# Kernel optimization log

Measured on AMD Instinct MI355X. Metric: run time of the kernel, lower is better.

Reference implementation:

```python
import jax, jax.numpy as jnp
import numpy as np

D_IN = 1024
D_OUT = 1024
NUM_HEADS = 16
HEAD_DIM = D_OUT // NUM_HEADS


def setup_inputs() -> dict:
    key = jax.random.key(0)
    ks = jax.random.split(key, 6)
    s = 1.0 / np.sqrt(D_IN)
    x = jax.random.normal(ks[0], (2, 2048, D_IN), dtype=jnp.float32)
    Wq = jax.random.uniform(ks[1], (D_IN, D_OUT), jnp.float32, -s, s)
    Wk = jax.random.uniform(ks[2], (D_IN, D_OUT), jnp.float32, -s, s)
    Wv = jax.random.uniform(ks[3], (D_IN, D_OUT), jnp.float32, -s, s)
    Wo = jax.random.uniform(ks[4], (D_OUT, D_OUT), jnp.float32, -s, s)
    bo = jax.random.uniform(ks[5], (D_OUT,), jnp.float32, -s, s)
    return {"x": x, "Wq": Wq, "Wk": Wk, "Wv": Wv, "Wo": Wo, "bo": bo}


def reference(x, Wq, Wk, Wv, Wo, bo):
    b, T, _ = x.shape
    # projections -> [b, heads, T, head_dim]
    def split_heads(y):
        return y.reshape(b, T, NUM_HEADS, HEAD_DIM).transpose(0, 2, 1, 3)
    q = split_heads(x @ Wq)
    k = split_heads(x @ Wk)
    v = split_heads(x @ Wv)
    scores = jnp.einsum("bhqd,bhkd->bhqk", q, k)  # [b,h,T,T]
    causal = jnp.triu(jnp.ones((T, T), dtype=bool), k=1)
    scores = jnp.where(causal, -jnp.inf, scores)
    weights = jax.nn.softmax(scores / np.sqrt(HEAD_DIM), axis=-1)
    # dropout p=0.0 (eval) -> identity
    ctx = jnp.einsum("bhqk,bhkd->bhqd", weights, v)
    ctx = ctx.transpose(0, 2, 1, 3).reshape(b, T, D_OUT)
    return ctx @ Wo + bo
```

## Files before the change

### kernel.cpp

```cpp
#include <hip/hip_runtime.h>
#include <hip/hip_bf16.h>
#include <math.h>

using f32x4  = __attribute__((ext_vector_type(4)))  float;
using f32x16 = __attribute__((ext_vector_type(16))) float;
using s16x8  = __attribute__((ext_vector_type(8)))  short;
using s16x4  = __attribute__((ext_vector_type(4)))  short;

#define HD 64
#define NH 16
#define TT 2048
#define DIN 1024
#define NB 2
#define M_TOK (NB*TT)
#define PADK 40
#define PSTR 36

__device__ __forceinline__ ushort f2b(float f) {
  union { float f; unsigned u; } v; v.f = f;
  unsigned u = v.u;
  return (ushort)((u + 0x7FFFu + ((u >> 16) & 1u)) >> 16);
}

__device__ __forceinline__ unsigned cvt_pk_bf16(float lo, float hi) {
  unsigned r;
  asm("v_cvt_pk_bf16_f32 %0, %1, %2" : "=v"(r) : "v"(lo), "v"(hi));
  return r;
}

__global__ __launch_bounds__(256) void cvt_f32_bf16(const float* __restrict__ in,
                                                    ushort* __restrict__ out, int n8) {
  int i = blockIdx.x * 256 + threadIdx.x;
  if (i >= n8) return;
  const f32x4* p = (const f32x4*)(in + (size_t)i * 8);
  f32x4 a = p[0], b = p[1];
  s16x8 o;
  o[0]=(short)f2b(a[0]); o[1]=(short)f2b(a[1]); o[2]=(short)f2b(a[2]); o[3]=(short)f2b(a[3]);
  o[4]=(short)f2b(b[0]); o[5]=(short)f2b(b[1]); o[6]=(short)f2b(b[2]); o[7]=(short)f2b(b[3]);
  *(s16x8*)(out + (size_t)i * 8) = o;
}

__global__ __launch_bounds__(256) void transpose_cvt(const float* __restrict__ W,
                                                     ushort* __restrict__ Wt, int K, int N) {
  __shared__ float tile[32][33];
  int nb = blockIdx.x * 32, kb = blockIdx.y * 32;
  int tx = threadIdx.x & 31, ty = threadIdx.x >> 5;
  #pragma unroll
  for (int j = ty; j < 32; j += 8) tile[j][tx] = W[(size_t)(kb + j) * N + nb + tx];
  __syncthreads();
  #pragma unroll
  for (int j = ty; j < 32; j += 8) Wt[(size_t)(nb + j) * K + kb + tx] = f2b(tile[tx][j]);
}

__global__ __launch_bounds__(256) void gemm_qkv(const ushort* __restrict__ Xb,
                                                const ushort* __restrict__ Wt,
                                                ushort* __restrict__ Qb,
                                                ushort* __restrict__ Kb,
                                                ushort* __restrict__ Vt) {
  __shared__ ushort Al[128 * PADK];
  __shared__ ushort Bl[128 * PADK];
  int tid = threadIdx.x, lane = tid & 63, wid = tid >> 6;
  int wr = wid >> 1, wc = wid & 1, g = lane >> 4, c = lane & 15;
  int m0 = blockIdx.y * 128, n0 = blockIdx.x * 128;
  f32x4 acc[4][4] = {};
  for (int k0 = 0; k0 < DIN; k0 += 32) {
    __syncthreads();
    #pragma unroll
    for (int j = 0; j < 2; ++j) {
      int ci = tid + j * 256;
      int row = ci >> 2, part = ci & 3;
      *(s16x8*)&Al[row * PADK + part * 8] =
          *(const s16x8*)&Xb[(size_t)(m0 + row) * DIN + k0 + part * 8];
      *(s16x8*)&Bl[row * PADK + part * 8] =
          *(const s16x8*)&Wt[(size_t)(n0 + row) * DIN + k0 + part * 8];
    }
    __syncthreads();
    s16x8 af[4], bfr[4];
    #pragma unroll
    for (int i = 0; i < 4; ++i) {
      af[i]  = *(const s16x8*)&Al[(wr * 64 + i * 16 + c) * PADK + g * 8];
      bfr[i] = *(const s16x8*)&Bl[(wc * 64 + i * 16 + c) * PADK + g * 8];
    }
    #pragma unroll
    for (int i = 0; i < 4; ++i)
      #pragma unroll
      for (int jn = 0; jn < 4; ++jn)
        acc[i][jn] = __builtin_amdgcn_mfma_f32_16x16x32_bf16(af[i], bfr[jn], acc[i][jn], 0, 0, 0);
  }
  #pragma unroll
  for (int i = 0; i < 4; ++i)
    #pragma unroll
    for (int jn = 0; jn < 4; ++jn) {
      int mrow = m0 + wr * 64 + i * 16 + g * 4;
      int n = n0 + wc * 64 + jn * 16 + c;
      int b = mrow >> 11, t = mrow & (TT - 1);
      int which = n >> 10, nn = n & 1023, h = nn >> 6, d = nn & 63;
      size_t bh = (size_t)(b * NH + h);
      if (which == 2) {
        s16x4 pk;
        pk[0]=(short)f2b(acc[i][jn][0]); pk[1]=(short)f2b(acc[i][jn][1]);
        pk[2]=(short)f2b(acc[i][jn][2]); pk[3]=(short)f2b(acc[i][jn][3]);
        *(s16x4*)&Vt[(bh * HD + d) * TT + t] = pk;
      } else {
        float sc = (which == 0) ? 0.125f * 1.44269504f : 1.0f;
        ushort* dst = (which == 0) ? &Qb[(bh * TT + t) * HD + d]
                                   : &Kb[(bh * TT + t) * HD + d];
        #pragma unroll
        for (int r = 0; r < 4; ++r) dst[(size_t)r * HD] = f2b(acc[i][jn][r] * sc);
      }
    }
}

__global__ __launch_bounds__(256, 4) void attn_fwd(const ushort* __restrict__ Qb,
                                                   const ushort* __restrict__ Kb,
                                                   const ushort* __restrict__ Vt,
                                                   ushort* __restrict__ Ctx) {
  __shared__ __align__(16) char smem[11264];
  int bh = blockIdx.y;
  int qc = (gridDim.x - 1) - blockIdx.x;
  int q0 = qc * 32;
  const ushort* Qh = Qb + (size_t)bh * TT * HD;
  const ushort* Kh = Kb + (size_t)bh * TT * HD;
  const ushort* Vh = Vt + (size_t)bh * HD * TT;
  int tid = threadIdx.x, lane = tid & 63, w = tid >> 6;
  int hi = lane >> 5, c32 = lane & 31;
  int q_abs = q0 + c32;
  int nt = qc + 1;

  ushort* pw = (ushort*)smem + w * (32 * PSTR);

  s16x8 qf[4];
  #pragma unroll
  for (int s = 0; s < 4; ++s)
    qf[s] = *(const s16x8*)&Qh[(size_t)q_abs * HD + s * 16 + 8 * hi];

  f32x16 cA[2] = {};
  float m = -INFINITY, l = 0.f;

  s16x8 kfc[4];
  {
    int tt = (w < nt) ? w : 0;
    #pragma unroll
    for (int s = 0; s < 4; ++s)
      kfc[s] = *(const s16x8*)&Kh[(size_t)(tt * 32 + c32) * HD + s * 16 + 8 * hi];
  }

  for (int t = w; t < nt; t += 4) {
    int kv0 = t * 32;
    s16x8 vf0[2], vf1[2];
    #pragma unroll
    for (int ks = 0; ks < 2; ++ks) {
      vf0[ks] = *(const s16x8*)&Vh[(size_t)c32 * TT + kv0 + ks * 16 + 8 * hi];
      vf1[ks] = *(const s16x8*)&Vh[(size_t)(32 + c32) * TT + kv0 + ks * 16 + 8 * hi];
    }
    f32x16 S = {};
    #pragma unroll
    for (int s = 0; s < 4; ++s)
      S = __builtin_amdgcn_mfma_f32_32x32x16_bf16(kfc[s], qf[s], S, 0, 0, 0);
    if (t + 4 < nt) {
      #pragma unroll
      for (int s = 0; s < 4; ++s)
        kfc[s] = *(const s16x8*)&Kh[(size_t)((t + 4) * 32 + c32) * HD + s * 16 + 8 * hi];
    }
    if (t == qc) {
      #pragma unroll
      for (int r = 0; r < 16; ++r) {
        int pat = (r & 3) + 8 * (r >> 2) + 4 * hi;
        S[r] = (pat > c32) ? -INFINITY : S[r];
      }
    }
    float mx[8];
    #pragma unroll
    for (int i = 0; i < 8; ++i) mx[i] = fmaxf(S[2 * i], S[2 * i + 1]);
    #pragma unroll
    for (int i = 0; i < 4; ++i) mx[i] = fmaxf(mx[i], mx[i + 4]);
    mx[0] = fmaxf(fmaxf(mx[0], mx[2]), fmaxf(mx[1], mx[3]));
    float tmax = fmaxf(mx[0], __shfl_xor(mx[0], 32));
    if (__any(tmax > m + 8.f)) {
      float mnew = fmaxf(m, tmax);
      float alpha = exp2f(m - mnew);
      l *= alpha;
      #pragma unroll
      for (int dt = 0; dt < 2; ++dt)
        #pragma unroll
        for (int r = 0; r < 16; ++r) cA[dt][r] *= alpha;
      m = mnew;
    }
    #pragma unroll
    for (int r = 0; r < 16; ++r) S[r] = exp2f(S[r] - m);
    float sm[8];
    #pragma unroll
    for (int i = 0; i < 8; ++i) sm[i] = S[2 * i] + S[2 * i + 1];
    #pragma unroll
    for (int i = 0; i < 4; ++i) sm[i] += sm[i + 4];
    float rsum = (sm[0] + sm[2]) + (sm[1] + sm[3]);
    rsum += __shfl_xor(rsum, 32);
    l += rsum;
    #pragma unroll
    for (int j = 0; j < 8; ++j) {
      int kvb = ((2 * j) & 3) + 8 * (j >> 1) + 4 * hi;
      *(unsigned*)&pw[c32 * PSTR + kvb] = cvt_pk_bf16(S[2 * j], S[2 * j + 1]);
    }
    asm volatile("s_waitcnt lgkmcnt(0)" ::: "memory");
    #pragma unroll
    for (int ks = 0; ks < 2; ++ks) {
      s16x8 pf = *(const s16x8*)&pw[c32 * PSTR + ks * 16 + 8 * hi];
      cA[0] = __builtin_amdgcn_mfma_f32_32x32x16_bf16(vf0[ks], pf, cA[0], 0, 0, 0);
      cA[1] = __builtin_amdgcn_mfma_f32_32x32x16_bf16(vf1[ks], pf, cA[1], 0, 0, 0);
    }
  }

  __syncthreads();
  float* cb = (float*)smem;
  float* mb = (float*)(smem + 10240);
  float* lb = mb + 128;
  if (!hi) { mb[w * 32 + c32] = m; lb[w * 32 + c32] = l; }
  __syncthreads();

  int q  = tid >> 3;
  int dp = (tid & 7) * 2;
  float ew[4];
  {
    float mw[4];
    #pragma unroll
    for (int ww = 0; ww < 4; ++ww) mw[ww] = mb[ww * 32 + q];
    float mG = fmaxf(fmaxf(mw[0], mw[1]), fmaxf(mw[2], mw[3]));
    float lt = 0.f;
    #pragma unroll
    for (int ww = 0; ww < 4; ++ww) {
      ew[ww] = exp2f(mw[ww] - mG);
      lt += ew[ww] * lb[ww * 32 + q];
    }
    float inv = 1.f / lt;
    #pragma unroll
    for (int ww = 0; ww < 4; ++ww) ew[ww] *= inv;
  }
  int b = bh >> 4, h = bh & 15;
  #pragma unroll
  for (int rd = 0; rd < 4; ++rd) {
    int dt = rd >> 1, rh = rd & 1;
    float* dstq = &cb[(size_t)(w * 32 + c32) * 20];
    f32x4 v0 = { cA[dt][rh * 8 + 0], cA[dt][rh * 8 + 1], cA[dt][rh * 8 + 2], cA[dt][rh * 8 + 3] };
    f32x4 v1 = { cA[dt][rh * 8 + 4], cA[dt][rh * 8 + 5], cA[dt][rh * 8 + 6], cA[dt][rh * 8 + 7] };
    *(f32x4*)&dstq[4 * hi]     = v0;
    *(f32x4*)&dstq[8 + 4 * hi] = v1;
    __syncthreads();
    float s0 = 0.f, s1 = 0.f;
    #pragma unroll
    for (int ww = 0; ww < 4; ++ww) {
      const float* src = &cb[(size_t)(ww * 32 + q) * 20 + dp];
      s0 += ew[ww] * src[0];
      s1 += ew[ww] * src[1];
    }
    int dcol = h * HD + 32 * dt + 16 * rh + dp;
    *(unsigned*)&Ctx[((size_t)(b * TT) + q0 + q) * DIN + dcol] = cvt_pk_bf16(s0, s1);
    if (rd < 3) __syncthreads();
  }
}

__global__ __launch_bounds__(256) void gemm_out(const ushort* __restrict__ Cb,
                                                const ushort* __restrict__ Wot,
                                                const float* __restrict__ bo,
                                                float* __restrict__ Out) {
  __shared__ ushort Al[128 * PADK];
  __shared__ ushort Bl[128 * PADK];
  int tid = threadIdx.x, lane = tid & 63, wid = tid >> 6;
  int wr = wid >> 1, wc = wid & 1, g = lane >> 4, c = lane & 15;
  int m0 = blockIdx.y * 128, n0 = blockIdx.x * 128;
  f32x4 acc[4][4] = {};
  for (int k0 = 0; k0 < DIN; k0 += 32) {
    __syncthreads();
    #pragma unroll
    for (int j = 0; j < 2; ++j) {
      int ci = tid + j * 256;
      int row = ci >> 2, part = ci & 3;
      *(s16x8*)&Al[row * PADK + part * 8] =
          *(const s16x8*)&Cb[(size_t)(m0 + row) * DIN + k0 + part * 8];
      *(s16x8*)&Bl[row * PADK + part * 8] =
          *(const s16x8*)&Wot[(size_t)(n0 + row) * DIN + k0 + part * 8];
    }
    __syncthreads();
    s16x8 af[4], bfr[4];
    #pragma unroll
    for (int i = 0; i < 4; ++i) {
      af[i]  = *(const s16x8*)&Al[(wr * 64 + i * 16 + c) * PADK + g * 8];
      bfr[i] = *(const s16x8*)&Bl[(wc * 64 + i * 16 + c) * PADK + g * 8];
    }
    #pragma unroll
    for (int i = 0; i < 4; ++i)
      #pragma unroll
      for (int jn = 0; jn < 4; ++jn)
        acc[i][jn] = __builtin_amdgcn_mfma_f32_16x16x32_bf16(af[i], bfr[jn], acc[i][jn], 0, 0, 0);
  }
  #pragma unroll
  for (int i = 0; i < 4; ++i)
    #pragma unroll
    for (int jn = 0; jn < 4; ++jn) {
      int mrow = m0 + wr * 64 + i * 16 + g * 4;
      int n = n0 + wc * 64 + jn * 16 + c;
      float bias = bo[n];
      float* dst = &Out[(size_t)mrow * DIN + n];
      #pragma unroll
      for (int r = 0; r < 4; ++r) dst[(size_t)r * DIN] = acc[i][jn][r] + bias;
    }
}

extern "C" void kernel_launch(void* const* d_in, const int* in_sizes, int n_in,
                              void* d_out, int out_size, void* d_ws, size_t ws_size,
                              hipStream_t stream) {
  const float* x  = (const float*)d_in[0];
  const float* Wq = (const float*)d_in[1];
  const float* Wk = (const float*)d_in[2];
  const float* Wv = (const float*)d_in[3];
  const float* Wo = (const float*)d_in[4];
  const float* bo = (const float*)d_in[5];
  float* Out = (float*)d_out;

  char* ws = (char*)d_ws;
  size_t off = 0;
  auto alloc = [&](size_t bytes) -> char* {
    char* p = ws + off;
    off += (bytes + 255) & ~(size_t)255;
    return p;
  };
  ushort* Xb  = (ushort*)alloc((size_t)M_TOK * DIN * 2);
  ushort* Wt3 = (ushort*)alloc((size_t)3 * 1024 * DIN * 2);
  ushort* Wot = (ushort*)alloc((size_t)1024 * 1024 * 2);
  ushort* Qb  = (ushort*)alloc((size_t)NB * NH * TT * HD * 2);
  ushort* Kb  = (ushort*)alloc((size_t)NB * NH * TT * HD * 2);
  ushort* Vt  = (ushort*)alloc((size_t)NB * NH * TT * HD * 2);
  ushort* Cb  = (ushort*)alloc((size_t)M_TOK * DIN * 2);

  cvt_f32_bf16<<<(M_TOK * DIN / 8 + 255) / 256, 256, 0, stream>>>(x, Xb, M_TOK * DIN / 8);
  dim3 tgrid(1024 / 32, 1024 / 32);
  transpose_cvt<<<tgrid, 256, 0, stream>>>(Wq, Wt3,                   1024, 1024);
  transpose_cvt<<<tgrid, 256, 0, stream>>>(Wk, Wt3 + 1024 * 1024,     1024, 1024);
  transpose_cvt<<<tgrid, 256, 0, stream>>>(Wv, Wt3 + 2 * 1024 * 1024, 1024, 1024);
  transpose_cvt<<<tgrid, 256, 0, stream>>>(Wo, Wot,                   1024, 1024);

  gemm_qkv<<<dim3(3072 / 128, M_TOK / 128), 256, 0, stream>>>(Xb, Wt3, Qb, Kb, Vt);
  attn_fwd<<<dim3(TT / 32, NB * NH), 256, 0, stream>>>(Qb, Kb, Vt, Cb);
  gemm_out<<<dim3(1024 / 128, M_TOK / 128), 256, 0, stream>>>(Cb, Wot, bo, Out);
}
```

Measured before the change: 275.2 us.

## Widen attention KV tile to 64, remap blocks per XCD, use permlane32 swap

Each wave in the attention kernel now handles a 64-key tile per iteration, computing two 32x32 score blocks and doing four PV MFMA steps. This halves the loop trip count and amortizes the per-iteration softmax bookkeeping and LDS round-trips over more MFMAs. The grid becomes 1D, and block indices are remapped so that each XCD works on a fixed set of heads, longest query chunks first, which should improve L2 locality of K/V. Cross-half reductions use permlane32_swap instead of a shuffle. Register and LDS use go up, and the occupancy hint drops from 4 to 2 blocks per CU. Diagonal tiles now also compute some fully masked work.

New measurement: 238.5 us. 13.3% less time.

```diff
diff --git a/kernel.cpp b/kernel.cpp
--- a/kernel.cpp
+++ b/kernel.cpp
@@ -6,6 +6,7 @@
 using f32x16 = __attribute__((ext_vector_type(16))) float;
 using s16x8  = __attribute__((ext_vector_type(8)))  short;
 using s16x4  = __attribute__((ext_vector_type(4)))  short;
+using u32x2  = __attribute__((ext_vector_type(2)))  unsigned;
 
 #define HD 64
 #define NH 16
@@ -14,7 +15,7 @@
 #define NB 2
 #define M_TOK (NB*TT)
 #define PADK 40
-#define PSTR 36
+#define PSTR2 68
 
 __device__ __forceinline__ ushort f2b(float f) {
   union { float f; unsigned u; } v; v.f = f;
@@ -26,6 +27,15 @@
   unsigned r;
   asm("v_cvt_pk_bf16_f32 %0, %1, %2" : "=v"(r) : "v"(lo), "v"(hi));
   return r;
+}
+
+__device__ __forceinline__ float xhalf_max(float v) {
+  u32x2 r = __builtin_amdgcn_permlane32_swap(__float_as_uint(v), __float_as_uint(v), false, false);
+  return fmaxf(__uint_as_float(r.x), __uint_as_float(r.y));
+}
+__device__ __forceinline__ float xhalf_sum(float v) {
+  u32x2 r = __builtin_amdgcn_permlane32_swap(__float_as_uint(v), __float_as_uint(v), false, false);
+  return __uint_as_float(r.x) + __uint_as_float(r.y);
 }
 
 __global__ __launch_bounds__(256) void cvt_f32_bf16(const float* __restrict__ in,
@@ -111,13 +121,15 @@
     }
 }
 
-__global__ __launch_bounds__(256, 4) void attn_fwd(const ushort* __restrict__ Qb,
+__global__ __launch_bounds__(256, 2) void attn_fwd(const ushort* __restrict__ Qb,
                                                    const ushort* __restrict__ Kb,
                                                    const ushort* __restrict__ Vt,
                                                    ushort* __restrict__ Ctx) {
-  __shared__ __align__(16) char smem[11264];
-  int bh = blockIdx.y;
-  int qc = (gridDim.x - 1) - blockIdx.x;
+  __shared__ __align__(16) char smem[17920];
+  int L = blockIdx.x;
+  int xcd = L & 7, j = L >> 3;
+  int bh = xcd + 8 * (j & 3);
+  int qc = 63 - (j >> 2);
   int q0 = qc * 32;
   const ushort* Qh = Qb + (size_t)bh * TT * HD;
   const ushort* Kh = Kb + (size_t)bh * TT * HD;
@@ -125,9 +137,9 @@
   int tid = threadIdx.x, lane = tid & 63, w = tid >> 6;
   int hi = lane >> 5, c32 = lane & 31;
   int q_abs = q0 + c32;
-  int nt = qc + 1;
-
-  ushort* pw = (ushort*)smem + w * (32 * PSTR);
+  int nt64 = (q0 + 32 + 63) >> 6;
+
+  ushort* pw = (ushort*)smem + w * (32 * PSTR2);
 
   s16x8 qf[4];
   #pragma unroll
@@ -137,45 +149,56 @@
   f32x16 cA[2] = {};
   float m = -INFINITY, l = 0.f;
 
-  s16x8 kfc[4];
+  s16x8 kfc[8];
   {
-    int tt = (w < nt) ? w : 0;
+    int tt = (w < nt64) ? w : 0;
+    #pragma unroll
+    for (int ss = 0; ss < 2; ++ss)
+      #pragma unroll
+      for (int s = 0; s < 4; ++s)
+        kfc[ss * 4 + s] =
+            *(const s16x8*)&Kh[(size_t)(tt * 64 + ss * 32 + c32) * HD + s * 16 + 8 * hi];
+  }
+
+  for (int t = w; t < nt64; t += 4) {
+    int kv0 = t * 64;
+    s16x8 vf[2][4];
+    #pragma unroll
+    for (int dt = 0; dt < 2; ++dt)
+      #pragma unroll
+      for (int ks = 0; ks < 4; ++ks)
+        vf[dt][ks] = *(const s16x8*)&Vh[(size_t)(dt * 32 + c32) * TT + kv0 + ks * 16 + 8 * hi];
+    f32x16 S0 = {}, S1 = {};
     #pragma unroll
     for (int s = 0; s < 4; ++s)
-      kfc[s] = *(const s16x8*)&Kh[(size_t)(tt * 32 + c32) * HD + s * 16 + 8 * hi];
-  }
-
-  for (int t = w; t < nt; t += 4) {
-    int kv0 = t * 32;
-    s16x8 vf0[2], vf1[2];
-    #pragma unroll
-    for (int ks = 0; ks < 2; ++ks) {
-      vf0[ks] = *(const s16x8*)&Vh[(size_t)c32 * TT + kv0 + ks * 16 + 8 * hi];
-      vf1[ks] = *(const s16x8*)&Vh[(size_t)(32 + c32) * TT + kv0 + ks * 16 + 8 * hi];
-    }
-    f32x16 S = {};
+      S0 = __builtin_amdgcn_mfma_f32_32x32x16_bf16(kfc[s], qf[s], S0, 0, 0, 0);
     #pragma unroll
     for (int s = 0; s < 4; ++s)
-      S = __builtin_amdgcn_mfma_f32_32x32x16_bf16(kfc[s], qf[s], S, 0, 0, 0);
-    if (t + 4 < nt) {
-      #pragma unroll
-      for (int s = 0; s < 4; ++s)
-        kfc[s] = *(const s16x8*)&Kh[(size_t)((t + 4) * 32 + c32) * HD + s * 16 + 8 * hi];
-    }
-    if (t == qc) {
+      S1 = __builtin_amdgcn_mfma_f32_32x32x16_bf16(kfc[4 + s], qf[s], S1, 0, 0, 0);
+    if (t + 4 < nt64) {
+      #pragma unroll
+      for (int ss = 0; ss < 2; ++ss)
+        #pragma unroll
+        for (int s = 0; s < 4; ++s)
+          kfc[ss * 4 + s] =
+              *(const s16x8*)&Kh[(size_t)((t + 4) * 64 + ss * 32 + c32) * HD + s * 16 + 8 * hi];
+    }
+    if (kv0 + 63 > q0) {
       #pragma unroll
       for (int r = 0; r < 16; ++r) {
-        int pat = (r & 3) + 8 * (r >> 2) + 4 * hi;
-        S[r] = (pat > c32) ? -INFINITY : S[r];
+        int base = kv0 + (r & 3) + 8 * (r >> 2) + 4 * hi;
+        S0[r] = (base > q_abs) ? -INFINITY : S0[r];
+        S1[r] = (base + 32 > q_abs) ? -INFINITY : S1[r];
       }
     }
     float mx[8];
     #pragma unroll
-    for (int i = 0; i < 8; ++i) mx[i] = fmaxf(S[2 * i], S[2 * i + 1]);
+    for (int i = 0; i < 8; ++i)
+      mx[i] = fmaxf(fmaxf(S0[2 * i], S0[2 * i + 1]), fmaxf(S1[2 * i], S1[2 * i + 1]));
     #pragma unroll
     for (int i = 0; i < 4; ++i) mx[i] = fmaxf(mx[i], mx[i + 4]);
     mx[0] = fmaxf(fmaxf(mx[0], mx[2]), fmaxf(mx[1], mx[3]));
-    float tmax = fmaxf(mx[0], __shfl_xor(mx[0], 32));
+    float tmax = xhalf_max(mx[0]);
     if (__any(tmax > m + 8.f)) {
       float mnew = fmaxf(m, tmax);
       float alpha = exp2f(m - mnew);
@@ -187,26 +210,27 @@
       m = mnew;
     }
     #pragma unroll
-    for (int r = 0; r < 16; ++r) S[r] = exp2f(S[r] - m);
+    for (int r = 0; r < 16; ++r) { S0[r] = exp2f(S0[r] - m); S1[r] = exp2f(S1[r] - m); }
     float sm[8];
     #pragma unroll
-    for (int i = 0; i < 8; ++i) sm[i] = S[2 * i] + S[2 * i + 1];
+    for (int i = 0; i < 8; ++i)
+      sm[i] = (S0[2 * i] + S0[2 * i + 1]) + (S1[2 * i] + S1[2 * i + 1]);
     #pragma unroll
     for (int i = 0; i < 4; ++i) sm[i] += sm[i + 4];
     float rsum = (sm[0] + sm[2]) + (sm[1] + sm[3]);
-    rsum += __shfl_xor(rsum, 32);
-    l += rsum;
-    #pragma unroll
-    for (int j = 0; j < 8; ++j) {
-      int kvb = ((2 * j) & 3) + 8 * (j >> 1) + 4 * hi;
-      *(unsigned*)&pw[c32 * PSTR + kvb] = cvt_pk_bf16(S[2 * j], S[2 * j + 1]);
+    l += xhalf_sum(rsum);
+    #pragma unroll
+    for (int jj = 0; jj < 8; ++jj) {
+      int kvb = ((2 * jj) & 3) + 8 * (jj >> 1) + 4 * hi;
+      *(unsigned*)&pw[c32 * PSTR2 + kvb]      = cvt_pk_bf16(S0[2 * jj], S0[2 * jj + 1]);
+      *(unsigned*)&pw[c32 * PSTR2 + 32 + kvb] = cvt_pk_bf16(S1[2 * jj], S1[2 * jj + 1]);
     }
     asm volatile("s_waitcnt lgkmcnt(0)" ::: "memory");
     #pragma unroll
-    for (int ks = 0; ks < 2; ++ks) {
-      s16x8 pf = *(const s16x8*)&pw[c32 * PSTR + ks * 16 + 8 * hi];
-      cA[0] = __builtin_amdgcn_mfma_f32_32x32x16_bf16(vf0[ks], pf, cA[0], 0, 0, 0);
-      cA[1] = __builtin_amdgcn_mfma_f32_32x32x16_bf16(vf1[ks], pf, cA[1], 0, 0, 0);
+    for (int ks = 0; ks < 4; ++ks) {
+      s16x8 pf = *(const s16x8*)&pw[c32 * PSTR2 + ks * 16 + 8 * hi];
+      cA[0] = __builtin_amdgcn_mfma_f32_32x32x16_bf16(vf[0][ks], pf, cA[0], 0, 0, 0);
+      cA[1] = __builtin_amdgcn_mfma_f32_32x32x16_bf16(vf[1][ks], pf, cA[1], 0, 0, 0);
     }
   }
 
@@ -339,6 +363,6 @@
   transpose_cvt<<<tgrid, 256, 0, stream>>>(Wo, Wot,                   1024, 1024);
 
   gemm_qkv<<<dim3(3072 / 128, M_TOK / 128), 256, 0, stream>>>(Xb, Wt3, Qb, Kb, Vt);
-  attn_fwd<<<dim3(TT / 32, NB * NH), 256, 0, stream>>>(Qb, Kb, Vt, Cb);
+  attn_fwd<<<2048, 256, 0, stream>>>(Qb, Kb, Vt, Cb);
   gemm_out<<<dim3(1024 / 128, M_TOK / 128), 256, 0, stream>>>(Cb, Wot, bo, Out);
 }
```
